# Optimization experiments

Hardware: AMD Instinct MI355X
Metric: run time of the kernel (lower is better)

The kernel has to match this reference:

```python
import jax, jax.numpy as jnp
import numpy as np

K = 2           # top-k experts
TEMP = 1.0      # router temperature


def setup_inputs() -> dict:
    key = jax.random.key(0)
    k0, k1, k2, k3 = jax.random.split(key, 4)
    B, T, C, E = 4, 8192, 1024, 64
    x = jax.random.normal(k0, (B, T, C), dtype=jnp.float32)
    cond = jax.random.normal(k1, (B, C), dtype=jnp.float32)
    # nn.Linear weights: gate (E, C), cond_proj (C, 2C)
    Wg = jax.random.normal(k2, (E, C), dtype=jnp.float32) * 0.02
    Wc = jax.random.normal(k3, (C, 2 * C), dtype=jnp.float32) * 0.02
    return {"x": x, "cond": cond, "Wg": Wg, "Wc": Wc}


def reference(x, cond, Wg, Wc):
    B, T, C = x.shape
    E = Wg.shape[0]
    # conditioning path: broadcast cond over tokens, concat, project
    c_exp = jnp.broadcast_to(cond[:, None, :], (B, T, C))
    hc = jnp.concatenate([x, c_exp], axis=-1)          # (B,T,2C)
    h = jnp.einsum('btd,cd->btc', hc, Wc)              # (B,T,C)
    logits = jnp.einsum('btc,ec->bte', h, Wg) * (1.0 / TEMP)  # (B,T,E)
    probs = jax.nn.softmax(logits, axis=-1)
    topk_vals, idx = jax.lax.top_k(logits, K)          # (B,T,K), sorted desc
    scores = jax.nn.softmax(topk_vals, axis=-1)
    # aux stats (no_grad in torch)
    importance = jax.lax.stop_gradient(jnp.mean(probs, axis=(0, 1)))  # (E,)
    counts = jnp.zeros((E,), probs.dtype).at[idx.reshape(-1)].add(1.0)
    load = counts / jnp.clip(jnp.sum(counts), 1.0)
    load = jax.lax.stop_gradient(load)
    return (idx, scores, probs, importance, load)
```

## Files before the change

### kernel.cpp

```cpp
#include <hip/hip_runtime.h>
#include <math.h>

#define B_    4
#define T_    8192
#define C_    1024
#define E_    64
#define NTOK  (B_*T_)
#define KSEL  2

#define OFF_IDX    0
#define OFF_SCORES (NTOK*KSEL)
#define OFF_PROBS  (2*NTOK*KSEL)
#define OFF_IMP    (OFF_PROBS + NTOK*E_)
#define OFF_LOAD   (OFF_IMP + E_)

#define WS_W64    0
#define WS_W32    1048576
#define WS_WTH    1310720
#define WS_WTL    1441792
#define WS_LB64   1572864
#define WS_LB32   1574912
#define WS_CNT    1575936
#define WS_LIST   1576448

#define REFINE_CAP 8192
#define REFINE_EPS 3e-4f

typedef __attribute__((ext_vector_type(8))) short short8;
typedef __attribute__((ext_vector_type(4))) float f32x4;

__global__ __launch_bounds__(256) void k_comb(const float* __restrict__ Wg,
                                              const float* __restrict__ Wc,
                                              double* __restrict__ w64) {
    __shared__ float wc_s[64 * 64];
    __shared__ float wg_s[64 * 64];
    const int tid   = threadIdx.x;
    const int e     = tid & 63;
    const int dg    = tid >> 6;
    const int dtile = (blockIdx.x & 31) * 64;
    const int cbase = (blockIdx.x >> 5) * 128;

    double acc[16];
#pragma unroll
    for (int i = 0; i < 16; ++i) acc[i] = 0.0;

    for (int cc = 0; cc < 128; cc += 64) {
        const int c0 = cbase + cc;
        __syncthreads();
#pragma unroll
        for (int k = 0; k < 4; ++k) {
            int li = tid + k * 256;
            int r = li >> 4, c4 = (li & 15) * 4;
            *(float4*)&wc_s[r * 64 + c4] =
                *(const float4*)&Wc[(size_t)(c0 + r) * 2048 + dtile + c4];
        }
#pragma unroll
        for (int k = 0; k < 4; ++k) {
            int li = tid + k * 256;
            int r = li >> 4, c4 = (li & 15) * 4;
            float4 v = *(const float4*)&Wg[(size_t)r * 1024 + c0 + c4];
            wg_s[(c4 + 0) * 64 + r] = v.x;
            wg_s[(c4 + 1) * 64 + r] = v.y;
            wg_s[(c4 + 2) * 64 + r] = v.z;
            wg_s[(c4 + 3) * 64 + r] = v.w;
        }
        __syncthreads();
        for (int c = 0; c < 64; ++c) {
            double wg = (double)wg_s[c * 64 + e];
            const float* wcrow = &wc_s[c * 64 + dg * 16];
#pragma unroll
            for (int i = 0; i < 16; ++i)
                acc[i] += wg * (double)wcrow[i];
        }
    }
#pragma unroll
    for (int i = 0; i < 16; ++i) {
        double* p = &w64[(size_t)(dtile + dg * 16 + i) * 64 + e];
#if __has_builtin(__builtin_amdgcn_global_atomic_fadd_f64)
        unsafeAtomicAdd(p, acc[i]);
#else
        atomicAdd(p, acc[i]);
#endif
    }
}

__global__ __launch_bounds__(256) void k_finalize(const double* __restrict__ w64,
                                                  const float* __restrict__ cond,
                                                  float* __restrict__ wcomb32,
                                                  short* __restrict__ wTh,
                                                  short* __restrict__ wTl,
                                                  double* __restrict__ lbias64,
                                                  float* __restrict__ lbias32) {
    const int tid = threadIdx.x;
    if (blockIdx.x < 64) {
        const int e = blockIdx.x;
        for (int d = tid; d < 1024; d += 256) {
            float f = (float)w64[(size_t)d * 64 + e];
            wcomb32[d * 64 + e] = f;
            unsigned u = __float_as_uint(f);
            short hi = (short)(u >> 16);
            float r = f - __uint_as_float(u & 0xFFFF0000u);
            short lo = (short)(__float_as_uint(r) >> 16);
            wTh[e * 1024 + d] = hi;
            wTl[e * 1024 + d] = lo;
        }
    } else {
        const int b = blockIdx.x - 64;
        const int e = tid & 63, part = tid >> 6;
        double acc = 0.0;
        const int d0 = part * 256;
        for (int d = d0; d < d0 + 256; ++d)
            acc += (double)cond[b * 1024 + d] * w64[(size_t)(1024 + d) * 64 + e];
        __shared__ double red[256];
        red[tid] = acc;
        __syncthreads();
        if (tid < 64) {
            double s = red[tid] + red[tid + 64] + red[tid + 128] + red[tid + 192];
            lbias64[b * 64 + tid] = s;
            lbias32[b * 64 + tid] = (float)s;
        }
    }
}

__device__ __forceinline__ void cvt_split8(const float* __restrict__ p,
                                           short8& h, short8& l) {
    float4 v0 = *(const float4*)p;
    float4 v1 = *(const float4*)(p + 4);
    float xv[8] = {v0.x, v0.y, v0.z, v0.w, v1.x, v1.y, v1.z, v1.w};
#pragma unroll
    for (int j = 0; j < 8; ++j) {
        unsigned u = __float_as_uint(xv[j]);
        h[j] = (short)(u >> 16);
        float r = xv[j] - __uint_as_float(u & 0xFFFF0000u);
        l[j] = (short)(__float_as_uint(r) >> 16);
    }
}

#define MT   64
#define XPAD 68

__global__ __launch_bounds__(256) void k_main(const float* __restrict__ x,
                                              const short* __restrict__ wTh,
                                              const short* __restrict__ wTl,
                                              const float* __restrict__ lbias32,
                                              float* __restrict__ out,
                                              unsigned int* __restrict__ ref_cnt,
                                              int* __restrict__ ref_list) {
    __shared__ float xs[MT * XPAD];
    __shared__ float invs[MT];
    __shared__ unsigned int cnts[E_];

    const int tid    = threadIdx.x;
    const int wid    = tid >> 6;
    const int lane   = tid & 63;
    const int nn     = lane & 15;
    const int q8     = (lane >> 4) * 8;
    const int token0 = blockIdx.x * MT;
    const int t0     = token0 + wid * 16;
    const int b      = token0 / T_;

    if (tid < E_) cnts[tid] = 0;

    f32x4 acc[4];
#pragma unroll
    for (int et = 0; et < 4; ++et) acc[et] = (f32x4){0.f, 0.f, 0.f, 0.f};

    const float* aptr = x + (size_t)(t0 + nn) * 1024 + q8;
#pragma unroll 2
    for (int k0 = 0; k0 < 1024; k0 += 32) {
        short8 ah, al;
        cvt_split8(aptr + k0, ah, al);
#pragma unroll
        for (int et = 0; et < 4; ++et) {
            const size_t boff = (size_t)(et * 16 + nn) * 1024 + k0 + q8;
            short8 bh = *(const short8*)(wTh + boff);
            short8 bl = *(const short8*)(wTl + boff);
            acc[et] = __builtin_amdgcn_mfma_f32_16x16x32_bf16(ah, bh, acc[et], 0, 0, 0);
            acc[et] = __builtin_amdgcn_mfma_f32_16x16x32_bf16(ah, bl, acc[et], 0, 0, 0);
            acc[et] = __builtin_amdgcn_mfma_f32_16x16x32_bf16(al, bh, acc[et], 0, 0, 0);
        }
    }

    const int q4 = (lane >> 4) * 4;
#pragma unroll
    for (int et = 0; et < 4; ++et) {
        float lb = lbias32[b * 64 + et * 16 + nn];
#pragma unroll
        for (int r = 0; r < 4; ++r) {
            int tok = wid * 16 + q4 + r;
            xs[tok * XPAD + et * 16 + nn] = acc[et][r] + lb;
        }
    }
    __syncthreads();

    if (tid < MT) {
        const int t = tid;
        float v1 = -1e30f, v2 = -1e30f, v3 = -1e30f;
        int i1 = 0, i2 = 0;
        for (int e = 0; e < E_; ++e) {
            float l = xs[t * XPAD + e];
            if (l > v1)      { v3 = v2; v2 = v1; i2 = i1; v1 = l; i1 = e; }
            else if (l > v2) { v3 = v2; v2 = l; i2 = e; }
            else if (l > v3) { v3 = l; }
        }
        float sum = 0.f;
        for (int e = 0; e < E_; ++e) {
            float ex = __expf(xs[t * XPAD + e] - v1);
            xs[t * XPAD + e] = ex;
            sum += ex;
        }
        invs[t] = 1.0f / sum;

        const int gt = token0 + t;
        float s1 = 1.0f / (1.0f + __expf(v2 - v1));
        *(float2*)&out[OFF_IDX + (size_t)gt * 2]    = make_float2((float)i1, (float)i2);
        *(float2*)&out[OFF_SCORES + (size_t)gt * 2] = make_float2(s1, 1.0f - s1);
        atomicAdd(&cnts[i1], 1u);
        atomicAdd(&cnts[i2], 1u);

        float g12 = v1 - v2, g23 = v2 - v3;
        float g = g12 < g23 ? g12 : g23;
        if (g < REFINE_EPS) {
            unsigned int pos = atomicAdd(ref_cnt, 1u);
            if (pos < REFINE_CAP) ref_list[pos] = gt;
        }
    }
    __syncthreads();

    float* probs = out + OFF_PROBS + (size_t)token0 * E_;
#pragma unroll
    for (int k = 0; k < 4; ++k) {
        int li4 = tid + k * 256;
        int tok = li4 >> 4;
        int c4 = (li4 & 15) << 2;
        float4 ex = *(const float4*)&xs[tok * XPAD + c4];
        float inv = invs[tok];
        *(float4*)&probs[(size_t)li4 * 4] =
            make_float4(ex.x * inv, ex.y * inv, ex.z * inv, ex.w * inv);
    }

    if (tid < E_) {
        const int e = tid;
        float s = 0.f;
        for (int t = 0; t < MT; ++t) s += xs[t * XPAD + e] * invs[t];
        atomicAdd(&out[OFF_IMP + e],  s * (1.0f / (float)NTOK));
        atomicAdd(&out[OFF_LOAD + e], (float)cnts[e] * (1.0f / (float)(NTOK * KSEL)));
    }
}

__global__ __launch_bounds__(256) void k_refine(const float* __restrict__ x,
                                                const float* __restrict__ wcomb32,
                                                const double* __restrict__ lbias64,
                                                const unsigned int* __restrict__ ref_cnt,
                                                const int* __restrict__ ref_list,
                                                float* __restrict__ out) {
    int wave = (int)((blockIdx.x * blockDim.x + threadIdx.x) >> 6);
    int lane = threadIdx.x & 63;
    unsigned int n = *ref_cnt;
    if (n > REFINE_CAP) n = REFINE_CAP;
    const int nwaves = (int)((gridDim.x * blockDim.x) >> 6);

    for (unsigned int wi = wave; wi < n; wi += nwaves) {
        const int gt = ref_list[wi];
        const int b = gt / T_;
        const float* xrow = x + (size_t)gt * C_;
        double a0 = 0.0, a1 = 0.0, a2 = 0.0, a3 = 0.0;
        for (int d = 0; d < C_; d += 4) {
            a0 += (double)xrow[d + 0] * (double)wcomb32[(d + 0) * 64 + lane];
            a1 += (double)xrow[d + 1] * (double)wcomb32[(d + 1) * 64 + lane];
            a2 += (double)xrow[d + 2] * (double)wcomb32[(d + 2) * 64 + lane];
            a3 += (double)xrow[d + 3] * (double)wcomb32[(d + 3) * 64 + lane];
        }
        double acc = ((a0 + a1) + (a2 + a3)) + lbias64[b * 64 + lane];

        double v = acc; int id = lane;
        for (int off = 32; off > 0; off >>= 1) {
            double ov = __shfl_xor(v, off, 64);
            int oid   = __shfl_xor(id, off, 64);
            if (ov > v || (ov == v && oid < id)) { v = ov; id = oid; }
        }
        double v1 = v; int i1 = id;
        v = (lane == i1) ? -1e300 : acc; id = lane;
        for (int off = 32; off > 0; off >>= 1) {
            double ov = __shfl_xor(v, off, 64);
            int oid   = __shfl_xor(id, off, 64);
            if (ov > v || (ov == v && oid < id)) { v = ov; id = oid; }
        }
        double v2 = v; int i2 = id;

        if (lane == 0) {
            float s1 = (float)(1.0 / (1.0 + exp(v2 - v1)));
            *(float2*)&out[OFF_IDX + (size_t)gt * 2]    = make_float2((float)i1, (float)i2);
            *(float2*)&out[OFF_SCORES + (size_t)gt * 2] = make_float2(s1, 1.0f - s1);
        }
    }
}

extern "C" void kernel_launch(void* const* d_in, const int* in_sizes, int n_in,
                              void* d_out, int out_size, void* d_ws, size_t ws_size,
                              hipStream_t stream) {
    const float* x    = (const float*)d_in[0];
    const float* cond = (const float*)d_in[1];
    const float* Wg   = (const float*)d_in[2];
    const float* Wc   = (const float*)d_in[3];
    float* out = (float*)d_out;
    char*  ws  = (char*)d_ws;

    double* w64     = (double*)(ws + WS_W64);
    float*  wcomb32 = (float*)(ws + WS_W32);
    short*  wTh     = (short*)(ws + WS_WTH);
    short*  wTl     = (short*)(ws + WS_WTL);
    double* lbias64 = (double*)(ws + WS_LB64);
    float*  lbias32 = (float*)(ws + WS_LB32);
    unsigned int* ref_cnt = (unsigned int*)(ws + WS_CNT);
    int*    ref_list = (int*)(ws + WS_LIST);

    hipMemsetAsync(w64, 0, 2048 * 64 * sizeof(double), stream);
    hipMemsetAsync(ref_cnt, 0, 4, stream);
    hipMemsetAsync(out + OFF_IMP, 0, 2 * E_ * sizeof(float), stream);

    k_comb<<<256, 256, 0, stream>>>(Wg, Wc, w64);
    k_finalize<<<68, 256, 0, stream>>>(w64, cond, wcomb32, wTh, wTl, lbias64, lbias32);
    k_main<<<NTOK / MT, 256, 0, stream>>>(x, wTh, wTl, lbias32, out, ref_cnt, ref_list);
    k_refine<<<256, 256, 0, stream>>>(x, wcomb32, lbias64, ref_cnt, ref_list, out);
}
```

Measured before the change: 387.7 us.

## Split-K across waves in main GEMM with pre-swizzled weight layout

```diff
diff --git a/kernel.cpp b/kernel.cpp
--- a/kernel.cpp
+++ b/kernel.cpp
@@ -16,8 +16,8 @@
 
 #define WS_W64    0
 #define WS_W32    1048576
-#define WS_WTH    1310720
-#define WS_WTL    1441792
+#define WS_BSWH   1310720
+#define WS_BSWL   1441792
 #define WS_LB64   1572864
 #define WS_LB32   1574912
 #define WS_CNT    1575936
@@ -31,7 +31,9 @@
 
 __global__ __launch_bounds__(256) void k_comb(const float* __restrict__ Wg,
                                               const float* __restrict__ Wc,
-                                              double* __restrict__ w64) {
+                                              double* __restrict__ w64,
+                                              float* __restrict__ out,
+                                              unsigned int* __restrict__ ref_cnt) {
     __shared__ float wc_s[64 * 64];
     __shared__ float wg_s[64 * 64];
     const int tid   = threadIdx.x;
@@ -39,6 +41,11 @@
     const int dg    = tid >> 6;
     const int dtile = (blockIdx.x & 31) * 64;
     const int cbase = (blockIdx.x >> 5) * 128;
+
+    if (blockIdx.x == 0) {
+        if (tid < 2 * E_) out[OFF_IMP + tid] = 0.f;
+        if (tid == 2 * E_) *ref_cnt = 0u;
+    }
 
     double acc[16];
 #pragma unroll
@@ -87,13 +94,14 @@
 __global__ __launch_bounds__(256) void k_finalize(const double* __restrict__ w64,
                                                   const float* __restrict__ cond,
                                                   float* __restrict__ wcomb32,
-                                                  short* __restrict__ wTh,
-                                                  short* __restrict__ wTl,
+                                                  short* __restrict__ bswH,
+                                                  short* __restrict__ bswL,
                                                   double* __restrict__ lbias64,
                                                   float* __restrict__ lbias32) {
     const int tid = threadIdx.x;
     if (blockIdx.x < 64) {
-        const int e = blockIdx.x;
+        const int e  = blockIdx.x;
+        const int et = e >> 4, nn = e & 15;
         for (int d = tid; d < 1024; d += 256) {
             float f = (float)w64[(size_t)d * 64 + e];
             wcomb32[d * 64 + e] = f;
@@ -101,8 +109,10 @@
             short hi = (short)(u >> 16);
             float r = f - __uint_as_float(u & 0xFFFF0000u);
             short lo = (short)(__float_as_uint(r) >> 16);
-            wTh[e * 1024 + d] = hi;
-            wTl[e * 1024 + d] = lo;
+            int kchunk = d >> 5, qsel = (d >> 3) & 3, j = d & 7;
+            int idx = ((kchunk * 4 + et) * 64 + qsel * 16 + nn) * 8 + j;
+            bswH[idx] = hi;
+            bswL[idx] = lo;
         }
     } else {
         const int b = blockIdx.x - 64;
@@ -136,17 +146,17 @@
     }
 }
 
-#define MT   64
-#define XPAD 68
-
-__global__ __launch_bounds__(256) void k_main(const float* __restrict__ x,
-                                              const short* __restrict__ wTh,
-                                              const short* __restrict__ wTl,
-                                              const float* __restrict__ lbias32,
-                                              float* __restrict__ out,
-                                              unsigned int* __restrict__ ref_cnt,
-                                              int* __restrict__ ref_list) {
-    __shared__ float xs[MT * XPAD];
+#define MT    32
+#define ROWP  65
+
+__global__ __launch_bounds__(256, 4) void k_main(const float* __restrict__ x,
+                                                 const short* __restrict__ bswH,
+                                                 const short* __restrict__ bswL,
+                                                 const float* __restrict__ lbias32,
+                                                 float* __restrict__ out,
+                                                 unsigned int* __restrict__ ref_cnt,
+                                                 int* __restrict__ ref_list) {
+    __shared__ float accbuf[4 * MT * ROWP];
     __shared__ float invs[MT];
     __shared__ unsigned int cnts[E_];
 
@@ -154,59 +164,78 @@
     const int wid    = tid >> 6;
     const int lane   = tid & 63;
     const int nn     = lane & 15;
-    const int q8     = (lane >> 4) * 8;
+    const int qsel   = lane >> 4;
     const int token0 = blockIdx.x * MT;
-    const int t0     = token0 + wid * 16;
-    const int b      = token0 / T_;
+    const int b      = token0 >> 13;
 
     if (tid < E_) cnts[tid] = 0;
 
-    f32x4 acc[4];
-#pragma unroll
-    for (int et = 0; et < 4; ++et) acc[et] = (f32x4){0.f, 0.f, 0.f, 0.f};
-
-    const float* aptr = x + (size_t)(t0 + nn) * 1024 + q8;
+    f32x4 acc[2][4];
+#pragma unroll
+    for (int m = 0; m < 2; ++m)
+#pragma unroll
+        for (int et = 0; et < 4; ++et) acc[m][et] = (f32x4){0.f, 0.f, 0.f, 0.f};
+
+    const float* a0 = x + (size_t)(token0 + nn) * 1024 + wid * 256 + qsel * 8;
+    const float* a1 = a0 + (size_t)16 * 1024;
+    const short* bh0 = bswH + ((size_t)(wid * 8) * 4) * 512 + lane * 8;
+    const short* bl0 = bswL + ((size_t)(wid * 8) * 4) * 512 + lane * 8;
+
 #pragma unroll 2
-    for (int k0 = 0; k0 < 1024; k0 += 32) {
-        short8 ah, al;
-        cvt_split8(aptr + k0, ah, al);
+    for (int kc = 0; kc < 8; ++kc) {
+        short8 ah0, al0, ah1, al1;
+        cvt_split8(a0 + kc * 32, ah0, al0);
+        cvt_split8(a1 + kc * 32, ah1, al1);
+        const short* bh = bh0 + (size_t)kc * 4 * 512;
+        const short* bl = bl0 + (size_t)kc * 4 * 512;
 #pragma unroll
         for (int et = 0; et < 4; ++et) {
-            const size_t boff = (size_t)(et * 16 + nn) * 1024 + k0 + q8;
-            short8 bh = *(const short8*)(wTh + boff);
-            short8 bl = *(const short8*)(wTl + boff);
-            acc[et] = __builtin_amdgcn_mfma_f32_16x16x32_bf16(ah, bh, acc[et], 0, 0, 0);
-            acc[et] = __builtin_amdgcn_mfma_f32_16x16x32_bf16(ah, bl, acc[et], 0, 0, 0);
-            acc[et] = __builtin_amdgcn_mfma_f32_16x16x32_bf16(al, bh, acc[et], 0, 0, 0);
-        }
-    }
-
-    const int q4 = (lane >> 4) * 4;
-#pragma unroll
-    for (int et = 0; et < 4; ++et) {
-        float lb = lbias32[b * 64 + et * 16 + nn];
-#pragma unroll
-        for (int r = 0; r < 4; ++r) {
-            int tok = wid * 16 + q4 + r;
-            xs[tok * XPAD + et * 16 + nn] = acc[et][r] + lb;
-        }
+            short8 b_h = *(const short8*)(bh + et * 512);
+            short8 b_l = *(const short8*)(bl + et * 512);
+            acc[0][et] = __builtin_amdgcn_mfma_f32_16x16x32_bf16(ah0, b_h, acc[0][et], 0, 0, 0);
+            acc[0][et] = __builtin_amdgcn_mfma_f32_16x16x32_bf16(ah0, b_l, acc[0][et], 0, 0, 0);
+            acc[0][et] = __builtin_amdgcn_mfma_f32_16x16x32_bf16(al0, b_h, acc[0][et], 0, 0, 0);
+            acc[1][et] = __builtin_amdgcn_mfma_f32_16x16x32_bf16(ah1, b_h, acc[1][et], 0, 0, 0);
+            acc[1][et] = __builtin_amdgcn_mfma_f32_16x16x32_bf16(ah1, b_l, acc[1][et], 0, 0, 0);
+            acc[1][et] = __builtin_amdgcn_mfma_f32_16x16x32_bf16(al1, b_h, acc[1][et], 0, 0, 0);
+        }
+    }
+
+    const int q4 = qsel * 4;
+#pragma unroll
+    for (int m = 0; m < 2; ++m)
+#pragma unroll
+        for (int et = 0; et < 4; ++et)
+#pragma unroll
+            for (int r = 0; r < 4; ++r)
+                accbuf[wid * (MT * ROWP) + (m * 16 + q4 + r) * ROWP + et * 16 + nn] =
+                    acc[m][et][r];
+    __syncthreads();
+
+    for (int li = tid; li < MT * E_; li += 256) {
+        int tok = li >> 6, e = li & 63;
+        int o = tok * ROWP + e;
+        float s = accbuf[o] + accbuf[MT * ROWP + o] + accbuf[2 * MT * ROWP + o] +
+                  accbuf[3 * MT * ROWP + o] + lbias32[b * 64 + e];
+        accbuf[o] = s;
     }
     __syncthreads();
 
     if (tid < MT) {
         const int t = tid;
+        const int base = t * ROWP;
         float v1 = -1e30f, v2 = -1e30f, v3 = -1e30f;
         int i1 = 0, i2 = 0;
         for (int e = 0; e < E_; ++e) {
-            float l = xs[t * XPAD + e];
+            float l = accbuf[base + e];
             if (l > v1)      { v3 = v2; v2 = v1; i2 = i1; v1 = l; i1 = e; }
             else if (l > v2) { v3 = v2; v2 = l; i2 = e; }
             else if (l > v3) { v3 = l; }
         }
         float sum = 0.f;
         for (int e = 0; e < E_; ++e) {
-            float ex = __expf(xs[t * XPAD + e] - v1);
-            xs[t * XPAD + e] = ex;
+            float ex = __expf(accbuf[base + e] - v1);
+            accbuf[base + e] = ex;
             sum += ex;
         }
         invs[t] = 1.0f / sum;
@@ -229,20 +258,21 @@
 
     float* probs = out + OFF_PROBS + (size_t)token0 * E_;
 #pragma unroll
-    for (int k = 0; k < 4; ++k) {
+    for (int k = 0; k < 2; ++k) {
         int li4 = tid + k * 256;
         int tok = li4 >> 4;
         int c4 = (li4 & 15) << 2;
-        float4 ex = *(const float4*)&xs[tok * XPAD + c4];
         float inv = invs[tok];
+        int o = tok * ROWP + c4;
         *(float4*)&probs[(size_t)li4 * 4] =
-            make_float4(ex.x * inv, ex.y * inv, ex.z * inv, ex.w * inv);
+            make_float4(accbuf[o] * inv, accbuf[o + 1] * inv,
+                        accbuf[o + 2] * inv, accbuf[o + 3] * inv);
     }
 
     if (tid < E_) {
         const int e = tid;
         float s = 0.f;
-        for (int t = 0; t < MT; ++t) s += xs[t * XPAD + e] * invs[t];
+        for (int t = 0; t < MT; ++t) s += accbuf[t * ROWP + e] * invs[t];
         atomicAdd(&out[OFF_IMP + e],  s * (1.0f / (float)NTOK));
         atomicAdd(&out[OFF_LOAD + e], (float)cnts[e] * (1.0f / (float)(NTOK * KSEL)));
     }
@@ -308,19 +338,17 @@
 
     double* w64     = (double*)(ws + WS_W64);
     float*  wcomb32 = (float*)(ws + WS_W32);
-    short*  wTh     = (short*)(ws + WS_WTH);
-    short*  wTl     = (short*)(ws + WS_WTL);
+    short*  bswH    = (short*)(ws + WS_BSWH);
+    short*  bswL    = (short*)(ws + WS_BSWL);
     double* lbias64 = (double*)(ws + WS_LB64);
     float*  lbias32 = (float*)(ws + WS_LB32);
     unsigned int* ref_cnt = (unsigned int*)(ws + WS_CNT);
     int*    ref_list = (int*)(ws + WS_LIST);
 
     hipMemsetAsync(w64, 0, 2048 * 64 * sizeof(double), stream);
-    hipMemsetAsync(ref_cnt, 0, 4, stream);
-    hipMemsetAsync(out + OFF_IMP, 0, 2 * E_ * sizeof(float), stream);
-
-    k_comb<<<256, 256, 0, stream>>>(Wg, Wc, w64);
-    k_finalize<<<68, 256, 0, stream>>>(w64, cond, wcomb32, wTh, wTl, lbias64, lbias32);
-    k_main<<<NTOK / MT, 256, 0, stream>>>(x, wTh, wTl, lbias32, out, ref_cnt, ref_list);
-    k_refine<<<256, 256, 0, stream>>>(x, wcomb32, lbias64, ref_cnt, ref_list, out);
-}
+
+    k_comb<<<256, 256, 0, stream>>>(Wg, Wc, w64, out, ref_cnt);
+    k_finalize<<<68, 256, 0, stream>>>(w64, cond, wcomb32, bswH, bswL, lbias64, lbias32);
+    k_main<<<NTOK / MT, 256, 0, stream>>>(x, bswH, bswL, lbias32, out, ref_cnt, ref_list);
+    k_refine<<<128, 256, 0, stream>>>(x, wcomb32, lbias64, ref_cnt, ref_list, out);
+}
```

Result: faster. 370.0 us (-4.6%).
